# Kernel optimization log

Measured on AMD Instinct MI355X. Metric: run time of the kernel, lower is better.

The kernel has to match this reference:

```python
import jax, jax.numpy as jnp
import numpy as np

# Dimensions
B, Cin, Nn, T = 16, 1, 1024, 12   # batch, input channels, nodes, timesteps
H = 128                            # d_model (hidden_dim)
S2 = 32                            # complex state modes = state_dim // 2 (S4D)
NL = 2                             # num_temporal_layers


def setup_inputs() -> dict:
    key = jax.random.key(0)
    ks = jax.random.split(key, 10)
    x = jax.random.normal(ks[0], (B, Cin, Nn, T), jnp.float32)
    # encoder Linear(Cin -> H)
    enc_W = jax.random.normal(ks[1], (Cin, H), jnp.float32) / np.sqrt(Cin)
    enc_b = jnp.zeros((H,), jnp.float32)
    # S4D layer params, stacked over NL layers
    log_A_real = jnp.log(0.5 * jnp.ones((NL, H, S2), jnp.float32))
    A_imag = jnp.broadcast_to(np.pi * jnp.arange(S2, dtype=jnp.float32), (NL, H, S2))
    C_re = jax.random.normal(ks[2], (NL, H, S2), jnp.float32)
    C_im = jax.random.normal(ks[3], (NL, H, S2), jnp.float32)
    log_dt = jax.random.uniform(ks[4], (NL, H), jnp.float32,
                                minval=np.log(1e-3), maxval=np.log(1e-1))
    D = jax.random.normal(ks[5], (NL, H), jnp.float32)
    # output mixing: Conv1d(H -> 2H, kernel 1) followed by GLU
    out_W = jax.random.normal(ks[6], (NL, 2 * H, H), jnp.float32) / np.sqrt(H)
    out_b = jnp.zeros((NL, 2 * H), jnp.float32)
    # post-norm LayerNorm over feature dim
    ln_g = jnp.ones((NL, H), jnp.float32)
    ln_b = jnp.zeros((NL, H), jnp.float32)
    # 1x1 conv2d shortcut (Cin -> H)
    sc_W = jax.random.normal(ks[7], (H, Cin), jnp.float32) / np.sqrt(Cin)
    sc_b = jnp.zeros((H,), jnp.float32)
    return dict(x=x, enc_W=enc_W, enc_b=enc_b, log_A_real=log_A_real,
                A_imag=A_imag, C_re=C_re, C_im=C_im, log_dt=log_dt, D=D,
                out_W=out_W, out_b=out_b, ln_g=ln_g, ln_b=ln_b,
                sc_W=sc_W, sc_b=sc_b)


def _s4d_kernel(log_A_real, A_imag, C_re, C_im, log_dt, L):
    # Diagonal SSM kernel (S4D, ZOH discretization), Vandermonde product.
    A = -jnp.exp(log_A_real) + 1j * A_imag          # (H, S2)
    dt = jnp.exp(log_dt)[:, None]                    # (H, 1)
    dtA = A * dt                                     # (H, S2)
    C = (C_re + 1j * C_im) * (jnp.exp(dtA) - 1.0) / A
    V = jnp.exp(dtA[..., None] * jnp.arange(L))      # (H, S2, L) Vandermonde
    return 2.0 * jnp.einsum('hn,hnl->hl', C, V).real  # (H, L)


def _causal_conv(u, k):
    # FFT-based causal convolution: u (BN, H, L), k (H, L)
    L = u.shape[-1]
    n = 2 * L
    Uf = jnp.fft.rfft(u, n=n)
    Kf = jnp.fft.rfft(k, n=n)
    return jnp.fft.irfft(Uf * Kf, n=n)[..., :L]


def reference(x, enc_W, enc_b, log_A_real, A_imag, C_re, C_im, log_dt, D,
              out_W, out_b, ln_g, ln_b, sc_W, sc_b):
    Bq, C_, N_, T_ = x.shape
    # (B, C, N, T) -> (B*N, T, C)
    u = jnp.transpose(x, (0, 2, 3, 1)).reshape(Bq * N_, T_, C_)
    h = u @ enc_W + enc_b                      # encoder -> (BN, T, H)
    h = jnp.transpose(h, (0, 2, 1))            # (BN, H, T)
    for l in range(NL):
        z = h
        k = _s4d_kernel(log_A_real[l], A_imag[l], C_re[l], C_im[l], log_dt[l], T_)
        y = _causal_conv(z, k) + D[l][:, None] * z
        y = jax.nn.gelu(y, approximate=False)
        y = jnp.einsum('oh,bht->bot', out_W[l], y) + out_b[l][:, None]
        y = y[:, :H] * jax.nn.sigmoid(y[:, H:])  # GLU over channel dim
        h = y + h                                 # residual
        # post-norm LayerNorm over feature (H) dim
        ht = jnp.transpose(h, (0, 2, 1))          # (BN, T, H)
        mu = ht.mean(-1, keepdims=True)
        var = ht.var(-1, keepdims=True)
        ht = (ht - mu) / jnp.sqrt(var + 1e-5) * ln_g[l] + ln_b[l]
        h = jnp.transpose(ht, (0, 2, 1))
    # (BN, H, T) -> (B, H, N, T)
    out = jnp.transpose(h, (0, 2, 1)).reshape(Bq, N_, T_, H)
    out = jnp.transpose(out, (0, 3, 1, 2))
    # 1x1 conv2d shortcut on original x
    skip = jnp.einsum('hc,bcnt->bhnt', sc_W, x) + sc_b[None, :, None, None]
    return out + skip
```

## Files before the change

### kernel.cpp

```cpp
#include <hip/hip_runtime.h>
#include <math.h>

#define S4_H   128
#define S4_HP  136
#define S4_T   12
#define S4_TT  48
#define S4_S2  32
#define S4_SEQ 4
#define S4_NL  2
#define S4_N   1024
#define S4_BN  (16 * 1024)

typedef float f4 __attribute__((ext_vector_type(4)));
typedef short s8v __attribute__((ext_vector_type(8)));

__device__ __forceinline__ unsigned short f2bf(float f) {
  unsigned int u = __builtin_bit_cast(unsigned int, f);
  u += 0x7fffu + ((u >> 16) & 1u);
  return (unsigned short)(u >> 16);
}

__device__ __forceinline__ float fast_gelu(float x) {
  const float u = 1.5957691216057308f * x * fmaf(0.044715f, x * x, 1.0f);
  return x * __builtin_amdgcn_rcpf(1.0f + __expf(-u));
}

__device__ __forceinline__ float fast_sigmoid(float g) {
  return __builtin_amdgcn_rcpf(1.0f + __expf(-g));
}

__device__ __forceinline__ void s4d_row(const float* __restrict__ log_A_real,
                                        const float* __restrict__ A_imag,
                                        const float* __restrict__ C_re,
                                        const float* __restrict__ C_im,
                                        const float* __restrict__ log_dt,
                                        int lh, float* kk) {
  const float dt = expf(log_dt[lh]);
#pragma unroll
  for (int t = 0; t < S4_T; ++t) kk[t] = 0.f;
  const int base = lh * S4_S2;
  for (int n = 0; n < S4_S2; ++n) {
    const float ar = -expf(log_A_real[base + n]);
    const float ai = A_imag[base + n];
    const float m  = expf(ar * dt);
    const float di = ai * dt;
    float sdi, cdi;
    sincosf(di, &sdi, &cdi);
    const float er = m * cdi, ei = m * sdi;
    const float inv = 1.0f / (ar * ar + ai * ai);
    const float x0 = er - 1.0f;
    const float qr = (x0 * ar + ei * ai) * inv;
    const float qi = (ei * ar - x0 * ai) * inv;
    const float c0r = C_re[base + n], c0i = C_im[base + n];
    const float cr = c0r * qr - c0i * qi;
    const float ci = c0r * qi + c0i * qr;
    float vr = 1.f, vi = 0.f;
#pragma unroll
    for (int t = 0; t < S4_T; ++t) {
      kk[t] = fmaf(cr, vr, fmaf(-ci, vi, kk[t]));
      const float nvr = vr * er - vi * ei;
      vi = vr * ei + vi * er;
      vr = nvr;
    }
  }
#pragma unroll
  for (int t = 0; t < S4_T; ++t) kk[t] *= 2.0f;
}

__global__ __launch_bounds__(256) void s4_prep(
    const float* __restrict__ oW, const float* __restrict__ lAr,
    const float* __restrict__ Aim, const float* __restrict__ Cre,
    const float* __restrict__ Cim, const float* __restrict__ ldt,
    unsigned short* __restrict__ Wbf, float* __restrict__ kout) {
  const int tid = blockIdx.x * 256 + (int)threadIdx.x;
  const int i = tid * 4;
  if (i < S4_NL * 2 * S4_H * S4_H) {
    const f4 v = *reinterpret_cast<const f4*>(&oW[i]);
    ushort4 o;
    o.x = f2bf(v[0]); o.y = f2bf(v[1]); o.z = f2bf(v[2]); o.w = f2bf(v[3]);
    *reinterpret_cast<ushort4*>(&Wbf[i]) = o;
  }
  if (tid < S4_NL * S4_H) {
    float kk[S4_T];
    s4d_row(lAr, Aim, Cre, Cim, ldt, tid, kk);
#pragma unroll
    for (int t = 0; t < S4_T; ++t) kout[tid * S4_T + t] = kk[t];
  }
}

__global__ __launch_bounds__(256, 3) void s4_mfma(
    const float* __restrict__ x, const float* __restrict__ enc_W,
    const float* __restrict__ enc_b, const float* __restrict__ Dp,
    const float* __restrict__ out_b, const float* __restrict__ ln_g,
    const float* __restrict__ ln_b, const float* __restrict__ sc_W,
    const float* __restrict__ sc_b, const unsigned short* __restrict__ Wbf,
    const float* __restrict__ kws, float* __restrict__ out) {
  __shared__ __align__(16) float hb[S4_TT][S4_HP];
  __shared__ __align__(16) unsigned short gb[S4_TT][S4_HP];
  __shared__ __align__(16) float xb[S4_SEQ][S4_T];

  const int tid  = threadIdx.x;
  const int seq0 = blockIdx.x * S4_SEQ;

  if (tid < S4_SEQ * S4_T) {
    const int s = tid / S4_T, t = tid - s * S4_T;
    xb[s][t] = x[(seq0 + s) * S4_T + t];
  }
  __syncthreads();

  {
    const int h = tid & (S4_H - 1);
    const float ew = enc_W[h], eb = enc_b[h];
#pragma unroll
    for (int sp = 0; sp < 2; ++sp) {
      const int s = (tid >> 7) + 2 * sp;
#pragma unroll
      for (int t = 0; t < S4_T; ++t)
        hb[s * S4_T + t][h] = fmaf(xb[s][t], ew, eb);
    }
  }

  for (int l = 0; l < S4_NL; ++l) {
    __syncthreads();
    {
      const int h = tid & (S4_H - 1);
      const float* kp = &kws[(l * S4_H + h) * S4_T];
      const f4 k0 = *(const f4*)(kp), k1 = *(const f4*)(kp + 4),
               k2 = *(const f4*)(kp + 8);
      const float kr[S4_T] = {k0[0], k0[1], k0[2], k0[3], k1[0], k1[1],
                              k1[2], k1[3], k2[0], k2[1], k2[2], k2[3]};
      const float dl = Dp[l * S4_H + h];
#pragma unroll
      for (int sp = 0; sp < 2; ++sp) {
        const int s = (tid >> 7) + 2 * sp;
        float z[S4_T];
#pragma unroll
        for (int t = 0; t < S4_T; ++t) z[t] = hb[s * S4_T + t][h];
#pragma unroll
        for (int t = 0; t < S4_T; ++t) {
          float a = dl * z[t];
#pragma unroll
          for (int ss = 0; ss <= t; ++ss) a = fmaf(kr[t - ss], z[ss], a);
          gb[s * S4_T + t][h] = f2bf(fast_gelu(a));
        }
      }
    }
    __syncthreads();
    {
      const int w = tid >> 6;
      const int lane = tid & 63;
      const int r = lane & 15;
      const int q = lane >> 4;
      f4 acc[2][2][3] = {};
#pragma unroll
      for (int p = 0; p < 2; ++p) {
        s8v af[2][4];
#pragma unroll
        for (int mi = 0; mi < 2; ++mi) {
          const int o = (2 * w + mi + p * 8) * 16 + r;
          const unsigned short* wp = &Wbf[(size_t)(l * 2 * S4_H + o) * S4_H + q * 8];
#pragma unroll
          for (int ks = 0; ks < 4; ++ks)
            af[mi][ks] = *reinterpret_cast<const s8v*>(wp + ks * 32);
        }
#pragma unroll
        for (int n = 0; n < 3; ++n) {
#pragma unroll
          for (int ks = 0; ks < 4; ++ks) {
            const s8v bfv =
                *reinterpret_cast<const s8v*>(&gb[n * 16 + r][ks * 32 + q * 8]);
#pragma unroll
            for (int mi = 0; mi < 2; ++mi)
              acc[p][mi][n] = __builtin_amdgcn_mfma_f32_16x16x32_bf16(
                  af[mi][ks], bfv, acc[p][mi][n], 0, 0, 0);
          }
        }
      }
#pragma unroll
      for (int mi = 0; mi < 2; ++mi) {
        const int oV = (2 * w + mi) * 16 + q * 4;
        const f4 bV = *(const f4*)&out_b[l * 2 * S4_H + oV];
        const f4 bG = *(const f4*)&out_b[l * 2 * S4_H + S4_H + oV];
#pragma unroll
        for (int n = 0; n < 3; ++n) {
          const int tt = n * 16 + r;
          f4* hp = reinterpret_cast<f4*>(&hb[tt][oV]);
          f4 hv = *hp;
#pragma unroll
          for (int j = 0; j < 4; ++j) {
            const float a = acc[0][mi][n][j] + bV[j];
            const float g = acc[1][mi][n][j] + bG[j];
            hv[j] += a * fast_sigmoid(g);
          }
          *hp = hv;
        }
      }
    }
    __syncthreads();
    {
      const int g = tid >> 2, q = tid & 3;
      if (g < S4_TT) {
        float s1 = 0.f, s2 = 0.f;
#pragma unroll
        for (int j = 0; j < 8; ++j) {
          const f4 v = *(const f4*)&hb[g][(q + 4 * j) * 4];
          s1 += v[0] + v[1] + v[2] + v[3];
          s2 = fmaf(v[0], v[0], s2); s2 = fmaf(v[1], v[1], s2);
          s2 = fmaf(v[2], v[2], s2); s2 = fmaf(v[3], v[3], s2);
        }
        s1 += __shfl_xor(s1, 1, 4); s1 += __shfl_xor(s1, 2, 4);
        s2 += __shfl_xor(s2, 1, 4); s2 += __shfl_xor(s2, 2, 4);
        const float mu   = s1 * (1.0f / S4_H);
        const float var  = s2 * (1.0f / S4_H) - mu * mu;
        const float rstd = rsqrtf(var + 1e-5f);
#pragma unroll
        for (int j = 0; j < 8; ++j) {
          const int e = (q + 4 * j) * 4;
          f4 v = *(const f4*)&hb[g][e];
          const f4 gg = *(const f4*)&ln_g[l * S4_H + e];
          const f4 bb = *(const f4*)&ln_b[l * S4_H + e];
#pragma unroll
          for (int jj = 0; jj < 4; ++jj)
            v[jj] = fmaf((v[jj] - mu) * rstd, gg[jj], bb[jj]);
          *(f4*)&hb[g][e] = v;
        }
      }
    }
  }
  __syncthreads();
  {
    const int h = tid & (S4_H - 1);
    const float sw = sc_W[h], sb = sc_b[h];
#pragma unroll
    for (int sp = 0; sp < 2; ++sp) {
      const int s = (tid >> 7) + 2 * sp;
      const int bn = seq0 + s;
      const int b = bn >> 10, n = bn & (S4_N - 1);
      float* op = out + (size_t)((b * S4_H + h) * S4_N + n) * S4_T;
#pragma unroll
      for (int qq = 0; qq < 3; ++qq) {
        f4 o;
#pragma unroll
        for (int t4 = 0; t4 < 4; ++t4) {
          const int t = qq * 4 + t4;
          o[t4] = hb[s * S4_T + t][h] + fmaf(sw, xb[s][t], sb);
        }
        *reinterpret_cast<f4*>(op + qq * 4) = o;
      }
    }
  }
}

__global__ __launch_bounds__(256) void s4_main_f32(
    const float* __restrict__ x, const float* __restrict__ enc_W,
    const float* __restrict__ enc_b, const float* __restrict__ log_A_real,
    const float* __restrict__ A_imag, const float* __restrict__ C_re,
    const float* __restrict__ C_im, const float* __restrict__ log_dt,
    const float* __restrict__ Dp, const float* __restrict__ out_W,
    const float* __restrict__ out_b, const float* __restrict__ ln_g,
    const float* __restrict__ ln_b, const float* __restrict__ sc_W,
    const float* __restrict__ sc_b, float* __restrict__ out) {
  __shared__ __align__(16) float hbuf[S4_SEQ][S4_H][S4_T];
  __shared__ __align__(16) float gbuf[S4_SEQ][S4_H][S4_T];
  __shared__ __align__(16) float kbuf[S4_NL][S4_H][S4_T];
  __shared__ __align__(16) float xbuf[S4_SEQ][S4_T];
  const int tid = threadIdx.x;
  const int seq0 = blockIdx.x * S4_SEQ;
  if (tid < S4_SEQ * S4_T) {
    const int s = tid / S4_T, t = tid - s * S4_T;
    xbuf[s][t] = x[(seq0 + s) * S4_T + t];
  }
  {
    float kk[S4_T];
    s4d_row(log_A_real, A_imag, C_re, C_im, log_dt, tid, kk);
#pragma unroll
    for (int t = 0; t < S4_T; ++t) (&kbuf[0][0][0])[tid * S4_T + t] = kk[t];
  }
  __syncthreads();
  for (int r = tid; r < S4_SEQ * S4_H; r += 256) {
    const int s = r >> 7, h = r & (S4_H - 1);
    const float ew = enc_W[h], eb = enc_b[h];
#pragma unroll
    for (int t = 0; t < S4_T; ++t) hbuf[s][h][t] = fmaf(xbuf[s][t], ew, eb);
  }
  for (int l = 0; l < S4_NL; ++l) {
    __syncthreads();
    for (int r = tid; r < S4_SEQ * S4_H; r += 256) {
      const int s = r >> 7, h = r & (S4_H - 1);
      float z[S4_T], kr[S4_T];
#pragma unroll
      for (int t = 0; t < S4_T; ++t) {
        z[t] = hbuf[s][h][t];
        kr[t] = kbuf[l][h][t];
      }
      const float dl = Dp[l * S4_H + h];
#pragma unroll
      for (int t = 0; t < S4_T; ++t) {
        float a = dl * z[t];
#pragma unroll
        for (int ss = 0; ss <= t; ++ss) a = fmaf(kr[t - ss], z[ss], a);
        gbuf[s][h][t] = 0.5f * a * (1.0f + erff(a * 0.70710678118654752f));
      }
    }
    __syncthreads();
    {
      const int op = tid & (S4_H - 1);
      const int sg = tid >> 7;
      const float* __restrict__ W0 = out_W + (size_t)(l * 2 * S4_H + op) * S4_H;
      const float* __restrict__ W1 = W0 + S4_H * S4_H;
      float acc0[2][S4_T], acc1[2][S4_T];
#pragma unroll
      for (int s2 = 0; s2 < 2; ++s2)
#pragma unroll
        for (int t = 0; t < S4_T; ++t) { acc0[s2][t] = 0.f; acc1[s2][t] = 0.f; }
      for (int h0 = 0; h0 < S4_H; h0 += 4) {
        const float4 w0 = *reinterpret_cast<const float4*>(W0 + h0);
        const float4 w1 = *reinterpret_cast<const float4*>(W1 + h0);
        const float w0a[4] = {w0.x, w0.y, w0.z, w0.w};
        const float w1a[4] = {w1.x, w1.y, w1.z, w1.w};
#pragma unroll
        for (int j = 0; j < 4; ++j) {
#pragma unroll
          for (int s2 = 0; s2 < 2; ++s2) {
            const float* gp = &gbuf[2 * sg + s2][h0 + j][0];
            const float4 ga = *reinterpret_cast<const float4*>(gp);
            const float4 gc = *reinterpret_cast<const float4*>(gp + 4);
            const float4 ge = *reinterpret_cast<const float4*>(gp + 8);
            const float gg[S4_T] = {ga.x, ga.y, ga.z, ga.w, gc.x, gc.y,
                                    gc.z, gc.w, ge.x, ge.y, ge.z, ge.w};
#pragma unroll
            for (int t = 0; t < S4_T; ++t) {
              acc0[s2][t] = fmaf(w0a[j], gg[t], acc0[s2][t]);
              acc1[s2][t] = fmaf(w1a[j], gg[t], acc1[s2][t]);
            }
          }
        }
      }
      const float b0 = out_b[l * 2 * S4_H + op];
      const float b1 = out_b[l * 2 * S4_H + S4_H + op];
#pragma unroll
      for (int s2 = 0; s2 < 2; ++s2) {
        const int seq = 2 * sg + s2;
#pragma unroll
        for (int t = 0; t < S4_T; ++t) {
          const float a = acc0[s2][t] + b0;
          const float g = acc1[s2][t] + b1;
          hbuf[seq][op][t] += a * (1.0f / (1.0f + expf(-g)));
        }
      }
    }
    __syncthreads();
    {
      const int col = tid >> 2;
      const int ing = tid & 3;
      if (col < S4_SEQ * S4_T) {
        const int s = col / S4_T, t = col - s * S4_T;
        float s1 = 0.f, s2v = 0.f;
#pragma unroll
        for (int i = 0; i < S4_H / 4; ++i) {
          const float v = hbuf[s][ing * 32 + i][t];
          s1 += v;
          s2v = fmaf(v, v, s2v);
        }
        s1 += __shfl_xor(s1, 1, 4); s1 += __shfl_xor(s1, 2, 4);
        s2v += __shfl_xor(s2v, 1, 4); s2v += __shfl_xor(s2v, 2, 4);
        const float mu = s1 * (1.0f / S4_H);
        const float var = s2v * (1.0f / S4_H) - mu * mu;
        const float rstd = rsqrtf(var + 1e-5f);
#pragma unroll
        for (int i = 0; i < S4_H / 4; ++i) {
          const int h = ing * 32 + i;
          const float v = hbuf[s][h][t];
          hbuf[s][h][t] =
              fmaf((v - mu) * rstd, ln_g[l * S4_H + h], ln_b[l * S4_H + h]);
        }
      }
    }
  }
  __syncthreads();
  for (int r = tid; r < S4_SEQ * S4_H; r += 256) {
    const int s = r >> 7, h = r & (S4_H - 1);
    const int bn = seq0 + s;
    const int b = bn >> 10, n = bn & (S4_N - 1);
    const float sw = sc_W[h], sb = sc_b[h];
#pragma unroll
    for (int q = 0; q < 3; ++q) {
      float4 o;
      const float4 hv0 = *reinterpret_cast<const float4*>(&hbuf[s][h][4 * q]);
      const float4 xv = *reinterpret_cast<const float4*>(&xbuf[s][4 * q]);
      o.x = hv0.x + fmaf(sw, xv.x, sb);
      o.y = hv0.y + fmaf(sw, xv.y, sb);
      o.z = hv0.z + fmaf(sw, xv.z, sb);
      o.w = hv0.w + fmaf(sw, xv.w, sb);
      reinterpret_cast<float4*>(out + (size_t)((b * S4_H + h) * S4_N + n) *
                                          S4_T)[q] = o;
    }
  }
}

extern "C" void kernel_launch(void* const* d_in, const int* in_sizes, int n_in,
                              void* d_out, int out_size, void* d_ws,
                              size_t ws_size, hipStream_t stream) {
  const float* x     = (const float*)d_in[0];
  const float* enc_W = (const float*)d_in[1];
  const float* enc_b = (const float*)d_in[2];
  const float* lAr   = (const float*)d_in[3];
  const float* Aim   = (const float*)d_in[4];
  const float* Cre   = (const float*)d_in[5];
  const float* Cim   = (const float*)d_in[6];
  const float* ldt   = (const float*)d_in[7];
  const float* Dp    = (const float*)d_in[8];
  const float* oW    = (const float*)d_in[9];
  const float* ob    = (const float*)d_in[10];
  const float* lg    = (const float*)d_in[11];
  const float* lb    = (const float*)d_in[12];
  const float* scW   = (const float*)d_in[13];
  const float* scb   = (const float*)d_in[14];
  float* out = (float*)d_out;

  const int grid = S4_BN / S4_SEQ;
  const size_t wbytes = (size_t)(S4_NL * 2 * S4_H * S4_H) * sizeof(unsigned short);
  const size_t kbytes = (size_t)(S4_NL * S4_H * S4_T) * sizeof(float);
  if (ws_size >= wbytes + kbytes) {
    unsigned short* Wbf = (unsigned short*)d_ws;
    float* kws = (float*)((char*)d_ws + wbytes);
    s4_prep<<<64, 256, 0, stream>>>(oW, lAr, Aim, Cre, Cim, ldt, Wbf, kws);
    s4_mfma<<<grid, 256, 0, stream>>>(x, enc_W, enc_b, Dp, ob, lg, lb, scW,
                                      scb, Wbf, kws, out);
  } else {
    s4_main_f32<<<grid, 256, 0, stream>>>(x, enc_W, enc_b, lAr, Aim, Cre, Cim,
                                          ldt, Dp, oW, ob, lg, lb, scW, scb,
                                          out);
  }
}
```

Baseline: 150.0 us.

## Defer LayerNorm apply into next-layer consumers and drop x staging buffer

The LayerNorm pass now only computes per-row mean and rstd into shared arrays. Normalization is applied lazily where the values are consumed: when the next layer reads its conv input, in the residual add of the GLU epilogue, and in the final output write. This removes a full read-modify-write sweep of the hidden buffer and one barrier per layer. x is loaded directly from global into registers instead of staged through shared memory, and the launch-bounds occupancy hint is raised from 3 to 4, which may add register pressure or spills.

```diff
diff --git a/kernel.cpp b/kernel.cpp
--- a/kernel.cpp
+++ b/kernel.cpp
@@ -24,7 +24,6 @@
   const float u = 1.5957691216057308f * x * fmaf(0.044715f, x * x, 1.0f);
   return x * __builtin_amdgcn_rcpf(1.0f + __expf(-u));
 }
-
 __device__ __forceinline__ float fast_sigmoid(float g) {
   return __builtin_amdgcn_rcpf(1.0f + __expf(-g));
 }
@@ -88,7 +87,7 @@
   }
 }
 
-__global__ __launch_bounds__(256, 3) void s4_mfma(
+__global__ __launch_bounds__(256, 4) void s4_mfma(
     const float* __restrict__ x, const float* __restrict__ enc_W,
     const float* __restrict__ enc_b, const float* __restrict__ Dp,
     const float* __restrict__ out_b, const float* __restrict__ ln_g,
@@ -97,51 +96,61 @@
     const float* __restrict__ kws, float* __restrict__ out) {
   __shared__ __align__(16) float hb[S4_TT][S4_HP];
   __shared__ __align__(16) unsigned short gb[S4_TT][S4_HP];
-  __shared__ __align__(16) float xb[S4_SEQ][S4_T];
+  __shared__ float smu[S4_TT];
+  __shared__ float srs[S4_TT];
 
   const int tid  = threadIdx.x;
   const int seq0 = blockIdx.x * S4_SEQ;
-
-  if (tid < S4_SEQ * S4_T) {
-    const int s = tid / S4_T, t = tid - s * S4_T;
-    xb[s][t] = x[(seq0 + s) * S4_T + t];
-  }
-  __syncthreads();
-
-  {
-    const int h = tid & (S4_H - 1);
-    const float ew = enc_W[h], eb = enc_b[h];
-#pragma unroll
-    for (int sp = 0; sp < 2; ++sp) {
-      const int s = (tid >> 7) + 2 * sp;
-#pragma unroll
-      for (int t = 0; t < S4_T; ++t)
-        hb[s * S4_T + t][h] = fmaf(xb[s][t], ew, eb);
-    }
-  }
+  const int hch  = tid & (S4_H - 1);
 
   for (int l = 0; l < S4_NL; ++l) {
-    __syncthreads();
     {
-      const int h = tid & (S4_H - 1);
-      const float* kp = &kws[(l * S4_H + h) * S4_T];
+      const float* kp = &kws[(l * S4_H + hch) * S4_T];
       const f4 k0 = *(const f4*)(kp), k1 = *(const f4*)(kp + 4),
                k2 = *(const f4*)(kp + 8);
       const float kr[S4_T] = {k0[0], k0[1], k0[2], k0[3], k1[0], k1[1],
                               k1[2], k1[3], k2[0], k2[1], k2[2], k2[3]};
-      const float dl = Dp[l * S4_H + h];
+      const float dl = Dp[l * S4_H + hch];
+      float z[2][S4_T];
+      if (l == 0) {
+        const float ew = enc_W[hch], eb = enc_b[hch];
+#pragma unroll
+        for (int sp = 0; sp < 2; ++sp) {
+          const int s = (tid >> 7) + 2 * sp;
+          const float* xp = x + (size_t)(seq0 + s) * S4_T;
+          const f4 x0 = *(const f4*)(xp), x1 = *(const f4*)(xp + 4),
+                   x2 = *(const f4*)(xp + 8);
+          const float xv[S4_T] = {x0[0], x0[1], x0[2], x0[3], x1[0], x1[1],
+                                  x1[2], x1[3], x2[0], x2[1], x2[2], x2[3]};
+#pragma unroll
+          for (int t = 0; t < S4_T; ++t) {
+            z[sp][t] = fmaf(xv[t], ew, eb);
+            hb[s * S4_T + t][hch] = z[sp][t];
+          }
+        }
+      } else {
+        const float lg = ln_g[(l - 1) * S4_H + hch];
+        const float lb = ln_b[(l - 1) * S4_H + hch];
+#pragma unroll
+        for (int sp = 0; sp < 2; ++sp) {
+          const int s = (tid >> 7) + 2 * sp;
+#pragma unroll
+          for (int t = 0; t < S4_T; ++t) {
+            const int tt = s * S4_T + t;
+            const float a = srs[tt] * lg;
+            z[sp][t] = fmaf(hb[tt][hch] - smu[tt], a, lb);
+          }
+        }
+      }
 #pragma unroll
       for (int sp = 0; sp < 2; ++sp) {
         const int s = (tid >> 7) + 2 * sp;
-        float z[S4_T];
-#pragma unroll
-        for (int t = 0; t < S4_T; ++t) z[t] = hb[s * S4_T + t][h];
 #pragma unroll
         for (int t = 0; t < S4_T; ++t) {
-          float a = dl * z[t];
-#pragma unroll
-          for (int ss = 0; ss <= t; ++ss) a = fmaf(kr[t - ss], z[ss], a);
-          gb[s * S4_T + t][h] = f2bf(fast_gelu(a));
+          float a = dl * z[sp][t];
+#pragma unroll
+          for (int ss = 0; ss <= t; ++ss) a = fmaf(kr[t - ss], z[sp][ss], a);
+          gb[s * S4_T + t][hch] = f2bf(fast_gelu(a));
         }
       }
     }
@@ -181,16 +190,25 @@
         const int oV = (2 * w + mi) * 16 + q * 4;
         const f4 bV = *(const f4*)&out_b[l * 2 * S4_H + oV];
         const f4 bG = *(const f4*)&out_b[l * 2 * S4_H + S4_H + oV];
+        f4 lgv = {1.f, 1.f, 1.f, 1.f}, lbv = {0.f, 0.f, 0.f, 0.f};
+        if (l > 0) {
+          lgv = *(const f4*)&ln_g[(l - 1) * S4_H + oV];
+          lbv = *(const f4*)&ln_b[(l - 1) * S4_H + oV];
+        }
 #pragma unroll
         for (int n = 0; n < 3; ++n) {
           const int tt = n * 16 + r;
+          float mu = 0.f, rs = 1.f;
+          if (l > 0) { mu = smu[tt]; rs = srs[tt]; }
           f4* hp = reinterpret_cast<f4*>(&hb[tt][oV]);
           f4 hv = *hp;
 #pragma unroll
           for (int j = 0; j < 4; ++j) {
             const float a = acc[0][mi][n][j] + bV[j];
             const float g = acc[1][mi][n][j] + bG[j];
-            hv[j] += a * fast_sigmoid(g);
+            const float res =
+                (l == 0) ? hv[j] : fmaf((hv[j] - mu) * rs, lgv[j], lbv[j]);
+            hv[j] = res + a * fast_sigmoid(g);
           }
           *hp = hv;
         }
@@ -210,41 +228,41 @@
         }
         s1 += __shfl_xor(s1, 1, 4); s1 += __shfl_xor(s1, 2, 4);
         s2 += __shfl_xor(s2, 1, 4); s2 += __shfl_xor(s2, 2, 4);
-        const float mu   = s1 * (1.0f / S4_H);
-        const float var  = s2 * (1.0f / S4_H) - mu * mu;
-        const float rstd = rsqrtf(var + 1e-5f);
-#pragma unroll
-        for (int j = 0; j < 8; ++j) {
-          const int e = (q + 4 * j) * 4;
-          f4 v = *(const f4*)&hb[g][e];
-          const f4 gg = *(const f4*)&ln_g[l * S4_H + e];
-          const f4 bb = *(const f4*)&ln_b[l * S4_H + e];
-#pragma unroll
-          for (int jj = 0; jj < 4; ++jj)
-            v[jj] = fmaf((v[jj] - mu) * rstd, gg[jj], bb[jj]);
-          *(f4*)&hb[g][e] = v;
-        }
-      }
-    }
-  }
-  __syncthreads();
+        const float mu  = s1 * (1.0f / S4_H);
+        const float var = s2 * (1.0f / S4_H) - mu * mu;
+        if (q == 0) {
+          smu[g] = mu;
+          srs[g] = rsqrtf(var + 1e-5f);
+        }
+      }
+    }
+    __syncthreads();
+  }
   {
-    const int h = tid & (S4_H - 1);
-    const float sw = sc_W[h], sb = sc_b[h];
+    const float sw = sc_W[hch], sb = sc_b[hch];
+    const float lg = ln_g[(S4_NL - 1) * S4_H + hch];
+    const float lb = ln_b[(S4_NL - 1) * S4_H + hch];
 #pragma unroll
     for (int sp = 0; sp < 2; ++sp) {
       const int s = (tid >> 7) + 2 * sp;
       const int bn = seq0 + s;
       const int b = bn >> 10, n = bn & (S4_N - 1);
-      float* op = out + (size_t)((b * S4_H + h) * S4_N + n) * S4_T;
+      const float* xp = x + (size_t)bn * S4_T;
+      const f4 x0 = *(const f4*)(xp), x1 = *(const f4*)(xp + 4),
+               x2 = *(const f4*)(xp + 8);
+      const float xv[S4_T] = {x0[0], x0[1], x0[2], x0[3], x1[0], x1[1],
+                              x1[2], x1[3], x2[0], x2[1], x2[2], x2[3]};
+      float ov[S4_T];
+#pragma unroll
+      for (int t = 0; t < S4_T; ++t) {
+        const int tt = s * S4_T + t;
+        ov[t] = fmaf((hb[tt][hch] - smu[tt]) * srs[tt], lg, lb) +
+                fmaf(sw, xv[t], sb);
+      }
+      float* op = out + (size_t)((b * S4_H + hch) * S4_N + n) * S4_T;
 #pragma unroll
       for (int qq = 0; qq < 3; ++qq) {
-        f4 o;
-#pragma unroll
-        for (int t4 = 0; t4 < 4; ++t4) {
-          const int t = qq * 4 + t4;
-          o[t4] = hb[s * S4_T + t][h] + fmaf(sw, xb[s][t], sb);
-        }
+        f4 o = {ov[4 * qq], ov[4 * qq + 1], ov[4 * qq + 2], ov[4 * qq + 3]};
         *reinterpret_cast<f4*>(op + qq * 4) = o;
       }
     }
```

Result: slower. 171.1 us (+14.1%).

## Halve sequences per block and raise occupancy target for MFMA kernel

Applied to the files above, without the earlier changes.

Each block now handles 2 sequences instead of 4, so each thread owns exactly one (sequence, channel) pair. The MFMA N dimension drops from 3 to 2 tiles with clamped reads and guarded writes for the padded rows. The launch bound asks for 8 blocks per CU instead of 3, and the encoder step is fused into the first layer's convolution pass, which removes a separate sync. The cost is twice as many blocks, each reloading the bf16 weight fragments from global/L2, plus MFMA work wasted on padded rows (24 valid of 32).

```diff
diff --git a/kernel.cpp b/kernel.cpp
--- a/kernel.cpp
+++ b/kernel.cpp
@@ -4,9 +4,9 @@
 #define S4_H   128
 #define S4_HP  136
 #define S4_T   12
-#define S4_TT  48
+#define S4_SEQ 2
+#define S4_TT  (S4_SEQ * S4_T)
 #define S4_S2  32
-#define S4_SEQ 4
 #define S4_NL  2
 #define S4_N   1024
 #define S4_BN  (16 * 1024)
@@ -24,7 +24,6 @@
   const float u = 1.5957691216057308f * x * fmaf(0.044715f, x * x, 1.0f);
   return x * __builtin_amdgcn_rcpf(1.0f + __expf(-u));
 }
-
 __device__ __forceinline__ float fast_sigmoid(float g) {
   return __builtin_amdgcn_rcpf(1.0f + __expf(-g));
 }
@@ -88,7 +87,7 @@
   }
 }
 
-__global__ __launch_bounds__(256, 3) void s4_mfma(
+__global__ __launch_bounds__(256, 8) void s4_mfma(
     const float* __restrict__ x, const float* __restrict__ enc_W,
     const float* __restrict__ enc_b, const float* __restrict__ Dp,
     const float* __restrict__ out_b, const float* __restrict__ ln_g,
@@ -101,6 +100,8 @@
 
   const int tid  = threadIdx.x;
   const int seq0 = blockIdx.x * S4_SEQ;
+  const int hch  = tid & (S4_H - 1);
+  const int sq   = tid >> 7;
 
   if (tid < S4_SEQ * S4_T) {
     const int s = tid / S4_T, t = tid - s * S4_T;
@@ -108,41 +109,32 @@
   }
   __syncthreads();
 
-  {
-    const int h = tid & (S4_H - 1);
-    const float ew = enc_W[h], eb = enc_b[h];
-#pragma unroll
-    for (int sp = 0; sp < 2; ++sp) {
-      const int s = (tid >> 7) + 2 * sp;
-#pragma unroll
-      for (int t = 0; t < S4_T; ++t)
-        hb[s * S4_T + t][h] = fmaf(xb[s][t], ew, eb);
-    }
-  }
-
   for (int l = 0; l < S4_NL; ++l) {
-    __syncthreads();
     {
-      const int h = tid & (S4_H - 1);
-      const float* kp = &kws[(l * S4_H + h) * S4_T];
+      const float* kp = &kws[(l * S4_H + hch) * S4_T];
       const f4 k0 = *(const f4*)(kp), k1 = *(const f4*)(kp + 4),
                k2 = *(const f4*)(kp + 8);
       const float kr[S4_T] = {k0[0], k0[1], k0[2], k0[3], k1[0], k1[1],
                               k1[2], k1[3], k2[0], k2[1], k2[2], k2[3]};
-      const float dl = Dp[l * S4_H + h];
-#pragma unroll
-      for (int sp = 0; sp < 2; ++sp) {
-        const int s = (tid >> 7) + 2 * sp;
-        float z[S4_T];
-#pragma unroll
-        for (int t = 0; t < S4_T; ++t) z[t] = hb[s * S4_T + t][h];
+      const float dl = Dp[l * S4_H + hch];
+      float z[S4_T];
+      if (l == 0) {
+        const float ew = enc_W[hch], eb = enc_b[hch];
 #pragma unroll
         for (int t = 0; t < S4_T; ++t) {
-          float a = dl * z[t];
-#pragma unroll
-          for (int ss = 0; ss <= t; ++ss) a = fmaf(kr[t - ss], z[ss], a);
-          gb[s * S4_T + t][h] = f2bf(fast_gelu(a));
-        }
+          z[t] = fmaf(xb[sq][t], ew, eb);
+          hb[sq * S4_T + t][hch] = z[t];
+        }
+      } else {
+#pragma unroll
+        for (int t = 0; t < S4_T; ++t) z[t] = hb[sq * S4_T + t][hch];
+      }
+#pragma unroll
+      for (int t = 0; t < S4_T; ++t) {
+        float a = dl * z[t];
+#pragma unroll
+        for (int ss = 0; ss <= t; ++ss) a = fmaf(kr[t - ss], z[ss], a);
+        gb[sq * S4_T + t][hch] = f2bf(fast_gelu(a));
       }
     }
     __syncthreads();
@@ -151,24 +143,27 @@
       const int lane = tid & 63;
       const int r = lane & 15;
       const int q = lane >> 4;
-      f4 acc[2][2][3] = {};
+      f4 acc[2][2][2] = {};
 #pragma unroll
       for (int p = 0; p < 2; ++p) {
         s8v af[2][4];
 #pragma unroll
         for (int mi = 0; mi < 2; ++mi) {
           const int o = (2 * w + mi + p * 8) * 16 + r;
-          const unsigned short* wp = &Wbf[(size_t)(l * 2 * S4_H + o) * S4_H + q * 8];
+          const unsigned short* wp =
+              &Wbf[(size_t)(l * 2 * S4_H + o) * S4_H + q * 8];
 #pragma unroll
           for (int ks = 0; ks < 4; ++ks)
             af[mi][ks] = *reinterpret_cast<const s8v*>(wp + ks * 32);
         }
 #pragma unroll
-        for (int n = 0; n < 3; ++n) {
+        for (int n = 0; n < 2; ++n) {
+          int brow = n * 16 + r;
+          if (brow > S4_TT - 1) brow = S4_TT - 1;
 #pragma unroll
           for (int ks = 0; ks < 4; ++ks) {
             const s8v bfv =
-                *reinterpret_cast<const s8v*>(&gb[n * 16 + r][ks * 32 + q * 8]);
+                *reinterpret_cast<const s8v*>(&gb[brow][ks * 32 + q * 8]);
 #pragma unroll
             for (int mi = 0; mi < 2; ++mi)
               acc[p][mi][n] = __builtin_amdgcn_mfma_f32_16x16x32_bf16(
@@ -182,17 +177,19 @@
         const f4 bV = *(const f4*)&out_b[l * 2 * S4_H + oV];
         const f4 bG = *(const f4*)&out_b[l * 2 * S4_H + S4_H + oV];
 #pragma unroll
-        for (int n = 0; n < 3; ++n) {
+        for (int n = 0; n < 2; ++n) {
           const int tt = n * 16 + r;
-          f4* hp = reinterpret_cast<f4*>(&hb[tt][oV]);
-          f4 hv = *hp;
-#pragma unroll
-          for (int j = 0; j < 4; ++j) {
-            const float a = acc[0][mi][n][j] + bV[j];
-            const float g = acc[1][mi][n][j] + bG[j];
-            hv[j] += a * fast_sigmoid(g);
+          if (tt < S4_TT) {
+            f4* hp = reinterpret_cast<f4*>(&hb[tt][oV]);
+            f4 hv = *hp;
+#pragma unroll
+            for (int j = 0; j < 4; ++j) {
+              const float a = acc[0][mi][n][j] + bV[j];
+              const float g = acc[1][mi][n][j] + bG[j];
+              hv[j] += a * fast_sigmoid(g);
+            }
+            *hp = hv;
           }
-          *hp = hv;
         }
       }
     }
@@ -226,31 +223,27 @@
         }
       }
     }
-  }
-  __syncthreads();
+    __syncthreads();
+  }
   {
-    const int h = tid & (S4_H - 1);
-    const float sw = sc_W[h], sb = sc_b[h];
-#pragma unroll
-    for (int sp = 0; sp < 2; ++sp) {
-      const int s = (tid >> 7) + 2 * sp;
-      const int bn = seq0 + s;
-      const int b = bn >> 10, n = bn & (S4_N - 1);
-      float* op = out + (size_t)((b * S4_H + h) * S4_N + n) * S4_T;
-#pragma unroll
-      for (int qq = 0; qq < 3; ++qq) {
-        f4 o;
-#pragma unroll
-        for (int t4 = 0; t4 < 4; ++t4) {
-          const int t = qq * 4 + t4;
-          o[t4] = hb[s * S4_T + t][h] + fmaf(sw, xb[s][t], sb);
-        }
-        *reinterpret_cast<f4*>(op + qq * 4) = o;
-      }
-    }
-  }
-}
-
+    const float sw = sc_W[hch], sb = sc_b[hch];
+    const int bn = seq0 + sq;
+    const int b = bn >> 10, n = bn & (S4_N - 1);
+    float* op = out + (size_t)((b * S4_H + hch) * S4_N + n) * S4_T;
+#pragma unroll
+    for (int qq = 0; qq < 3; ++qq) {
+      f4 o;
+#pragma unroll
+      for (int t4 = 0; t4 < 4; ++t4) {
+        const int t = qq * 4 + t4;
+        o[t4] = hb[sq * S4_T + t][hch] + fmaf(sw, xb[sq][t], sb);
+      }
+      *reinterpret_cast<f4*>(op + qq * 4) = o;
+    }
+  }
+}
+
+#define S4F_SEQ 4
 __global__ __launch_bounds__(256) void s4_main_f32(
     const float* __restrict__ x, const float* __restrict__ enc_W,
     const float* __restrict__ enc_b, const float* __restrict__ log_A_real,
@@ -260,13 +253,13 @@
     const float* __restrict__ out_b, const float* __restrict__ ln_g,
     const float* __restrict__ ln_b, const float* __restrict__ sc_W,
     const float* __restrict__ sc_b, float* __restrict__ out) {
-  __shared__ __align__(16) float hbuf[S4_SEQ][S4_H][S4_T];
-  __shared__ __align__(16) float gbuf[S4_SEQ][S4_H][S4_T];
+  __shared__ __align__(16) float hbuf[S4F_SEQ][S4_H][S4_T];
+  __shared__ __align__(16) float gbuf[S4F_SEQ][S4_H][S4_T];
   __shared__ __align__(16) float kbuf[S4_NL][S4_H][S4_T];
-  __shared__ __align__(16) float xbuf[S4_SEQ][S4_T];
+  __shared__ __align__(16) float xbuf[S4F_SEQ][S4_T];
   const int tid = threadIdx.x;
-  const int seq0 = blockIdx.x * S4_SEQ;
-  if (tid < S4_SEQ * S4_T) {
+  const int seq0 = blockIdx.x * S4F_SEQ;
+  if (tid < S4F_SEQ * S4_T) {
     const int s = tid / S4_T, t = tid - s * S4_T;
     xbuf[s][t] = x[(seq0 + s) * S4_T + t];
   }
@@ -277,7 +270,7 @@
     for (int t = 0; t < S4_T; ++t) (&kbuf[0][0][0])[tid * S4_T + t] = kk[t];
   }
   __syncthreads();
-  for (int r = tid; r < S4_SEQ * S4_H; r += 256) {
+  for (int r = tid; r < S4F_SEQ * S4_H; r += 256) {
     const int s = r >> 7, h = r & (S4_H - 1);
     const float ew = enc_W[h], eb = enc_b[h];
 #pragma unroll
@@ -285,7 +278,7 @@
   }
   for (int l = 0; l < S4_NL; ++l) {
     __syncthreads();
-    for (int r = tid; r < S4_SEQ * S4_H; r += 256) {
+    for (int r = tid; r < S4F_SEQ * S4_H; r += 256) {
       const int s = r >> 7, h = r & (S4_H - 1);
       float z[S4_T], kr[S4_T];
 #pragma unroll
@@ -353,7 +346,7 @@
     {
       const int col = tid >> 2;
       const int ing = tid & 3;
-      if (col < S4_SEQ * S4_T) {
+      if (col < S4F_SEQ * S4_T) {
         const int s = col / S4_T, t = col - s * S4_T;
         float s1 = 0.f, s2v = 0.f;
 #pragma unroll
@@ -378,7 +371,7 @@
     }
   }
   __syncthreads();
-  for (int r = tid; r < S4_SEQ * S4_H; r += 256) {
+  for (int r = tid; r < S4F_SEQ * S4_H; r += 256) {
     const int s = r >> 7, h = r & (S4_H - 1);
     const int bn = seq0 + s;
     const int b = bn >> 10, n = bn & (S4_N - 1);
@@ -418,18 +411,17 @@
   const float* scb   = (const float*)d_in[14];
   float* out = (float*)d_out;
 
-  const int grid = S4_BN / S4_SEQ;
   const size_t wbytes = (size_t)(S4_NL * 2 * S4_H * S4_H) * sizeof(unsigned short);
   const size_t kbytes = (size_t)(S4_NL * S4_H * S4_T) * sizeof(float);
   if (ws_size >= wbytes + kbytes) {
     unsigned short* Wbf = (unsigned short*)d_ws;
     float* kws = (float*)((char*)d_ws + wbytes);
     s4_prep<<<64, 256, 0, stream>>>(oW, lAr, Aim, Cre, Cim, ldt, Wbf, kws);
-    s4_mfma<<<grid, 256, 0, stream>>>(x, enc_W, enc_b, Dp, ob, lg, lb, scW,
-                                      scb, Wbf, kws, out);
+    s4_mfma<<<S4_BN / S4_SEQ, 256, 0, stream>>>(x, enc_W, enc_b, Dp, ob, lg,
+                                                lb, scW, scb, Wbf, kws, out);
   } else {
-    s4_main_f32<<<grid, 256, 0, stream>>>(x, enc_W, enc_b, lAr, Aim, Cre, Cim,
-                                          ldt, Dp, oW, ob, lg, lb, scW, scb,
-                                          out);
-  }
-}
+    s4_main_f32<<<S4_BN / S4F_SEQ, 256, 0, stream>>>(
+        x, enc_W, enc_b, lAr, Aim, Cre, Cim, ldt, Dp, oW, ob, lg, lb, scW,
+        scb, out);
+  }
+}
```

New measurement: 218.1 us. 45.4% more time.
